# Kernel optimization log

Hardware: AMD Instinct MI355X
Metric: run time of the kernel (lower is better)

## Reference

```python
import jax, jax.numpy as jnp
import numpy as np

B, S, I, H, NC = 256, 1024, 64, 128, 10

def setup_inputs() -> dict:
    key = jax.random.key(0)
    ks = jax.random.split(key, 12)
    s_dh = 1.0 / np.sqrt(I)
    s_lstm = 1.0 / np.sqrt(H)
    return {
        "values": jax.random.normal(ks[0], (B, S, I), dtype=jnp.float32),
        "masks": jax.random.randint(ks[1], (B, S, I), 0, 2, dtype=jnp.int32),
        "deltas": jax.random.uniform(ks[2], (B, S, I), dtype=jnp.float32),
        "W_dh": jax.random.uniform(ks[3], (H, I), minval=-s_dh, maxval=s_dh),
        "b_dh": jax.random.uniform(ks[4], (H,), minval=-s_dh, maxval=s_dh),
        "W_dx": jax.random.uniform(ks[5], (I, I), minval=-s_dh, maxval=s_dh),
        "b_dx": jax.random.uniform(ks[6], (I,), minval=-s_dh, maxval=s_dh),
        "W_ih": jax.random.uniform(ks[7], (4 * H, 2 * I), minval=-s_lstm, maxval=s_lstm),
        "W_hh": jax.random.uniform(ks[8], (4 * H, H), minval=-s_lstm, maxval=s_lstm),
        "b_ih": jax.random.uniform(ks[9], (4 * H,), minval=-s_lstm, maxval=s_lstm),
        "b_hh": jax.random.uniform(ks[10], (4 * H,), minval=-s_lstm, maxval=s_lstm),
        "W_out": jax.random.uniform(ks[11], (NC, H), minval=-s_lstm, maxval=s_lstm),
        "b_out": jnp.zeros((NC,), dtype=jnp.float32),
    }

def _grud_forward(values, masks_f, deltas, W_dh, b_dh, W_dx, b_dx, W_ih, W_hh, b_ih, b_hh, W_out, b_out):
    eye = jnp.eye(W_dx.shape[0], dtype=W_dx.dtype)
    W_dx_diag = W_dx * eye  # TemporalDecay diag=True masks weight with identity

    def step(carry, xs):
        h, c = carry
        x, m, d = xs  # each (B, I)
        gamma_h = jnp.exp(-jax.nn.relu(d @ W_dh.T + b_dh))  # (B, H)
        gamma_x = jnp.exp(-jax.nn.relu(d @ W_dx_diag.T + b_dx))  # (B, I)
        h = h * gamma_h
        x_h = m * x + (1.0 - m) * (1.0 - gamma_x)  # forwards=None -> f = 1.0
        inp = jnp.concatenate([x_h, m], axis=1)  # (B, 2I)
        gates = inp @ W_ih.T + b_ih + h @ W_hh.T + b_hh  # (B, 4H)
        i_g, f_g, g_g, o_g = jnp.split(gates, 4, axis=1)
        c = jax.nn.sigmoid(f_g) * c + jax.nn.sigmoid(i_g) * jnp.tanh(g_g)
        h = jax.nn.sigmoid(o_g) * jnp.tanh(c)
        return (h, c), x_h

    b, _, _ = values.shape
    hdim = W_hh.shape[1]
    h0 = jnp.zeros((b, hdim), dtype=values.dtype)
    c0 = jnp.zeros((b, hdim), dtype=values.dtype)
    xs = (jnp.swapaxes(values, 0, 1), jnp.swapaxes(masks_f, 0, 1), jnp.swapaxes(deltas, 0, 1))
    (h, c), imputes = jax.lax.scan(step, (h0, c0), xs)
    impute_tensor = jnp.swapaxes(imputes, 0, 1)  # (B, S, I)
    y_h = h @ W_out.T + b_out  # dropout is identity in eval mode
    return y_h, impute_tensor

def reference(values, masks, deltas, W_dh, b_dh, W_dx, b_dx, W_ih, W_hh, b_ih, b_hh, W_out, b_out):
    masks_f = masks.astype(values.dtype)
    return _grud_forward(values, masks_f, deltas, W_dh, b_dh, W_dx, b_dx, W_ih, W_hh, b_ih, b_hh, W_out, b_out)
```

## Files before the change

### kernel.cpp

```cpp
#include <hip/hip_runtime.h>
#include <hip/hip_fp16.h>

#define NB   256
#define NS   1024
#define NI   64
#define NH   128
#define NCLS 10

typedef _Float16 h1;
typedef h1 h2 __attribute__((ext_vector_type(2)));
struct alignas(16) H8 { h2 v[4]; };

__device__ __forceinline__ h2 mk2(float a, float b) {
  h2 r; r[0] = (h1)a; r[1] = (h1)b; return r;
}

__device__ __forceinline__ float fdot2(h2 a, h2 b, float c) {
#if __has_builtin(__builtin_amdgcn_fdot2)
  return __builtin_amdgcn_fdot2(a, b, c, false);
#else
  return c + (float)a[0] * (float)b[0] + (float)a[1] * (float)b[1];
#endif
}

__device__ __forceinline__ float fast_rcp(float x) {
#if __has_builtin(__builtin_amdgcn_rcpf)
  return __builtin_amdgcn_rcpf(x);
#else
  return 1.0f / x;
#endif
}

__device__ __forceinline__ float tanh_f(float x) {
  return 2.f * fast_rcp(1.f + __expf(-2.f * x)) - 1.f;
}

__device__ __forceinline__ float sigm(float x) {
  return fast_rcp(1.f + __expf(-x));
}

template<int CTRL>
__device__ __forceinline__ float dpp_add(float x) {
  int y = __builtin_amdgcn_update_dpp(0, __float_as_int(x), CTRL, 0xF, 0xF, true);
  return x + __int_as_float(y);
}
__device__ __forceinline__ float red8(float x) {
  x = dpp_add<0xB1>(x);
  x = dpp_add<0x4E>(x);
  x = dpp_add<0x141>(x);
  return x;
}

__global__ __launch_bounds__(1024, 4) void grud_fused(
    const float* __restrict__ values,
    const int*   __restrict__ masks,
    const float* __restrict__ deltas,
    const float* __restrict__ W_dh, const float* __restrict__ b_dh,
    const float* __restrict__ W_dx, const float* __restrict__ b_dx,
    const float* __restrict__ W_ih, const float* __restrict__ W_hh,
    const float* __restrict__ b_ih, const float* __restrict__ b_hh,
    const float* __restrict__ W_out, const float* __restrict__ b_out,
    float* __restrict__ out)
{
  const int b   = blockIdx.x;
  const int tid = threadIdx.x;
  const int l   = tid & 63;
  const int w   = tid >> 6;
  const int q   = l & 7;
  const int g   = l >> 3;
  const int j   = (w << 3) | g;
  const int e0  = q << 5;

  __shared__ alignas(16) h1 opA[256];
  __shared__ alignas(16) h1 opB[256];
  __shared__ float hfin[NH];

  h2 wt0[16], wt1[16], wt2[16], wt3[16];
  {
    const size_t roff = (e0 < 128) ? (size_t)e0 : (size_t)(e0 - 128);
    const float* wbase = (e0 < 128) ? W_ih : W_hh;
#define LOADW(WT, R)                                                          \
    {                                                                         \
      const float4* w4 = reinterpret_cast<const float4*>(                     \
          wbase + ((size_t)((R) * NH + j)) * 128 + roff);                     \
      _Pragma("unroll")                                                       \
      for (int k = 0; k < 8; ++k) {                                           \
        float4 f = w4[k];                                                     \
        WT[2 * k]     = mk2(f.x, f.y);                                        \
        WT[2 * k + 1] = mk2(f.z, f.w);                                        \
      }                                                                       \
    }
    LOADW(wt0, 0) LOADW(wt1, 1) LOADW(wt2, 2) LOADW(wt3, 3)
#undef LOADW
  }
  const float bs0 = b_ih[j]            + b_hh[j];
  const float bs1 = b_ih[NH + j]       + b_hh[NH + j];
  const float bs2 = b_ih[2 * NH + j]   + b_hh[2 * NH + j];
  const float bs3 = b_ih[3 * NH + j]   + b_hh[3 * NH + j];
  h2 wd0, wd1, wd2, wd3;
  {
    const float4* a4 = reinterpret_cast<const float4*>(W_dh + j * 64 + q * 8);
    float4 f0 = a4[0], f1 = a4[1];
    wd0 = mk2(f0.x, f0.y); wd1 = mk2(f0.z, f0.w);
    wd2 = mk2(f1.x, f1.y); wd3 = mk2(f1.z, f1.w);
  }
  const float bdh = b_dh[j];
  float wdx_i = 0.f, bdx_i = 0.f;
  if (tid < NI) { wdx_i = W_dx[tid * 64 + tid]; bdx_i = b_dx[tid]; }

  const size_t base_b = (size_t)b * NS * NI;
  float* out_y   = out;
  float* out_imp = out + NB * NCLS;

  if (tid < NH) opA[128 + tid] = (h1)0.f;
  if (tid < NI) {
    float x0 = values[base_b + tid];
    float m0 = (float)masks[base_b + tid];
    float d0 = deltas[base_b + tid];
    float gx = __expf(-fmaxf(d0 * wdx_i + bdx_i, 0.f));
    float xh = m0 * x0 + (1.f - m0) * (1.f - gx);
    out_imp[base_b + tid] = xh;
    opA[tid]      = (h1)xh;
    opA[64 + tid] = (h1)m0;
  }

  h1* cur = opA;
  h1* nxt = opB;
  float c_st = 0.f, h_st = 0.f;

  for (int t = 0; t < NS; ++t) {
    __syncthreads();
    const int    tn = (t + 1 < NS) ? (t + 1) : (NS - 1);
    const size_t nb = base_b + (size_t)tn * NI;

    const float4* dn4 = reinterpret_cast<const float4*>(deltas + nb + q * 8);
    float4 pa = dn4[0], pb = dn4[1];
    float px = 0.f, pm = 0.f, pdv = 0.f;
    if (tid < NI) {
      px  = values[nb + tid];
      pm  = (float)masks[nb + tid];
      pdv = deltas[nb + tid];
    }

    const H8* s4 = reinterpret_cast<const H8*>(cur + e0);
    H8 o0 = s4[0], o1 = s4[1], o2 = s4[2], o3 = s4[3];

    float a0 = 0.f, a1 = 0.f, a2 = 0.f, a3 = 0.f;
#pragma unroll
    for (int p = 0; p < 4; ++p) {
      a0 = fdot2(o0.v[p], wt0[p], a0);
      a1 = fdot2(o0.v[p], wt1[p], a1);
      a2 = fdot2(o0.v[p], wt2[p], a2);
      a3 = fdot2(o0.v[p], wt3[p], a3);
    }
#pragma unroll
    for (int p = 0; p < 4; ++p) {
      a0 = fdot2(o1.v[p], wt0[4 + p], a0);
      a1 = fdot2(o1.v[p], wt1[4 + p], a1);
      a2 = fdot2(o1.v[p], wt2[4 + p], a2);
      a3 = fdot2(o1.v[p], wt3[4 + p], a3);
    }
#pragma unroll
    for (int p = 0; p < 4; ++p) {
      a0 = fdot2(o2.v[p], wt0[8 + p], a0);
      a1 = fdot2(o2.v[p], wt1[8 + p], a1);
      a2 = fdot2(o2.v[p], wt2[8 + p], a2);
      a3 = fdot2(o2.v[p], wt3[8 + p], a3);
    }
#pragma unroll
    for (int p = 0; p < 4; ++p) {
      a0 = fdot2(o3.v[p], wt0[12 + p], a0);
      a1 = fdot2(o3.v[p], wt1[12 + p], a1);
      a2 = fdot2(o3.v[p], wt2[12 + p], a2);
      a3 = fdot2(o3.v[p], wt3[12 + p], a3);
    }

    float gi = red8(a0) + bs0;
    float gf = red8(a1) + bs1;
    float gg = red8(a2) + bs2;
    float go = red8(a3) + bs3;

    float ia = sigm(gi);
    float fa = sigm(gf);
    float ga = tanh_f(gg);
    float oa = sigm(go);

    c_st = fa * c_st + ia * ga;
    h_st = oa * tanh_f(c_st);

    h2 p0 = mk2(pa.x, pa.y), p1 = mk2(pa.z, pa.w);
    h2 p2 = mk2(pb.x, pb.y), p3 = mk2(pb.z, pb.w);
    float part = fdot2(p3, wd3, fdot2(p2, wd2, fdot2(p1, wd1, fdot2(p0, wd0, 0.f))));
    part = red8(part);
    float gh = __expf(-fmaxf(part + bdh, 0.f));

    if (tid < NI) {
      float gx = __expf(-fmaxf(pdv * wdx_i + bdx_i, 0.f));
      float xh = pm * px + (1.f - pm) * (1.f - gx);
      if (t + 1 < NS) out_imp[nb + tid] = xh;
      nxt[tid]      = (h1)xh;
      nxt[64 + tid] = (h1)pm;
    }
    if (q == 0) nxt[128 + j] = (h1)(h_st * gh);

    h1* tmp = cur; cur = nxt; nxt = tmp;
  }

  if (q == 0) hfin[j] = h_st;
  __syncthreads();
  if (tid < NCLS) {
    float acc = b_out[tid];
    const float4* wo4 = reinterpret_cast<const float4*>(W_out + tid * NH);
#pragma unroll
    for (int k = 0; k < 32; ++k) {
      float4 a = wo4[k];
      acc += a.x * hfin[4 * k] + a.y * hfin[4 * k + 1] +
             a.z * hfin[4 * k + 2] + a.w * hfin[4 * k + 3];
    }
    out_y[b * NCLS + tid] = acc;
  }
}

extern "C" void kernel_launch(void* const* d_in, const int* in_sizes, int n_in,
                              void* d_out, int out_size, void* d_ws, size_t ws_size,
                              hipStream_t stream) {
  (void)in_sizes; (void)n_in; (void)d_ws; (void)ws_size; (void)out_size;
  grud_fused<<<dim3(NB), dim3(1024), 0, stream>>>(
      (const float*)d_in[0],  (const int*)d_in[1],   (const float*)d_in[2],
      (const float*)d_in[3],  (const float*)d_in[4], (const float*)d_in[5],
      (const float*)d_in[6],  (const float*)d_in[7], (const float*)d_in[8],
      (const float*)d_in[9],  (const float*)d_in[10],(const float*)d_in[11],
      (const float*)d_in[12], (float*)d_out);
}
```

Measured before the change: 1.503 ms.

## Split each hidden unit across 4 lanes with 512-thread blocks and padded LDS

Each hidden unit now uses 4 lanes instead of 8, so blocks shrink from 1024 to 512 threads. Each lane holds 128 fp16 weights across the four gates, and the cross-lane reduction drops to two DPP steps. The LDS operand buffer is padded to 72-element chunks to cut bank conflicts on the wider per-lane reads, and the float-to-half conversion now uses packed cvt_pkrtz. The longer per-lane dot-product chain and higher register use may offset the cheaper barriers and reductions.

```diff
diff --git a/kernel.cpp b/kernel.cpp
--- a/kernel.cpp
+++ b/kernel.cpp
@@ -11,8 +11,11 @@
 typedef h1 h2 __attribute__((ext_vector_type(2)));
 struct alignas(16) H8 { h2 v[4]; };
 
-__device__ __forceinline__ h2 mk2(float a, float b) {
-  h2 r; r[0] = (h1)a; r[1] = (h1)b; return r;
+#define CH_H1  72
+#define BUF_H1 (4 * CH_H1)
+
+__device__ __forceinline__ h2 pk(float a, float b) {
+  return __builtin_bit_cast(h2, __builtin_amdgcn_cvt_pkrtz(a, b));
 }
 
 __device__ __forceinline__ float fdot2(h2 a, h2 b, float c) {
@@ -34,7 +37,6 @@
 __device__ __forceinline__ float tanh_f(float x) {
   return 2.f * fast_rcp(1.f + __expf(-2.f * x)) - 1.f;
 }
-
 __device__ __forceinline__ float sigm(float x) {
   return fast_rcp(1.f + __expf(-x));
 }
@@ -44,14 +46,13 @@
   int y = __builtin_amdgcn_update_dpp(0, __float_as_int(x), CTRL, 0xF, 0xF, true);
   return x + __int_as_float(y);
 }
-__device__ __forceinline__ float red8(float x) {
+__device__ __forceinline__ float red4(float x) {
   x = dpp_add<0xB1>(x);
   x = dpp_add<0x4E>(x);
-  x = dpp_add<0x141>(x);
   return x;
 }
 
-__global__ __launch_bounds__(1024, 4) void grud_fused(
+__global__ __launch_bounds__(512, 2) void grud_fused(
     const float* __restrict__ values,
     const int*   __restrict__ masks,
     const float* __restrict__ deltas,
@@ -66,45 +67,42 @@
   const int tid = threadIdx.x;
   const int l   = tid & 63;
   const int w   = tid >> 6;
-  const int q   = l & 7;
-  const int g   = l >> 3;
-  const int j   = (w << 3) | g;
-  const int e0  = q << 5;
-
-  __shared__ alignas(16) h1 opA[256];
-  __shared__ alignas(16) h1 opB[256];
+  const int q   = l & 3;
+  const int u   = (w << 4) | (l >> 2);
+
+  __shared__ alignas(16) h1 opA[BUF_H1];
+  __shared__ alignas(16) h1 opB[BUF_H1];
   __shared__ float hfin[NH];
 
-  h2 wt0[16], wt1[16], wt2[16], wt3[16];
+  h2 wt[4][32];
+#pragma unroll
+  for (int g = 0; g < 4; ++g) {
+    const int row = g * NH + u;
+    const float* src = (q < 2) ? (W_ih + (size_t)row * 128 + 64 * q)
+                               : (W_hh + (size_t)row * 128 + 64 * (q - 2));
+    const float4* s4 = reinterpret_cast<const float4*>(src);
+#pragma unroll
+    for (int k = 0; k < 16; ++k) {
+      float4 f = s4[k];
+      wt[g][2 * k]     = pk(f.x, f.y);
+      wt[g][2 * k + 1] = pk(f.z, f.w);
+    }
+  }
+  const float bs0 = 0.25f * (b_ih[u]          + b_hh[u]);
+  const float bs1 = 0.25f * (b_ih[NH + u]     + b_hh[NH + u]);
+  const float bs2 = 0.25f * (b_ih[2 * NH + u] + b_hh[2 * NH + u]);
+  const float bs3 = 0.25f * (b_ih[3 * NH + u] + b_hh[3 * NH + u]);
+  h2 wdh[8];
   {
-    const size_t roff = (e0 < 128) ? (size_t)e0 : (size_t)(e0 - 128);
-    const float* wbase = (e0 < 128) ? W_ih : W_hh;
-#define LOADW(WT, R)                                                          \
-    {                                                                         \
-      const float4* w4 = reinterpret_cast<const float4*>(                     \
-          wbase + ((size_t)((R) * NH + j)) * 128 + roff);                     \
-      _Pragma("unroll")                                                       \
-      for (int k = 0; k < 8; ++k) {                                           \
-        float4 f = w4[k];                                                     \
-        WT[2 * k]     = mk2(f.x, f.y);                                        \
-        WT[2 * k + 1] = mk2(f.z, f.w);                                        \
-      }                                                                       \
-    }
-    LOADW(wt0, 0) LOADW(wt1, 1) LOADW(wt2, 2) LOADW(wt3, 3)
-#undef LOADW
-  }
-  const float bs0 = b_ih[j]            + b_hh[j];
-  const float bs1 = b_ih[NH + j]       + b_hh[NH + j];
-  const float bs2 = b_ih[2 * NH + j]   + b_hh[2 * NH + j];
-  const float bs3 = b_ih[3 * NH + j]   + b_hh[3 * NH + j];
-  h2 wd0, wd1, wd2, wd3;
-  {
-    const float4* a4 = reinterpret_cast<const float4*>(W_dh + j * 64 + q * 8);
-    float4 f0 = a4[0], f1 = a4[1];
-    wd0 = mk2(f0.x, f0.y); wd1 = mk2(f0.z, f0.w);
-    wd2 = mk2(f1.x, f1.y); wd3 = mk2(f1.z, f1.w);
-  }
-  const float bdh = b_dh[j];
+    const float4* a4 = reinterpret_cast<const float4*>(W_dh + u * 64 + 16 * q);
+#pragma unroll
+    for (int k = 0; k < 4; ++k) {
+      float4 f = a4[k];
+      wdh[2 * k]     = pk(f.x, f.y);
+      wdh[2 * k + 1] = pk(f.z, f.w);
+    }
+  }
+  const float bdh4 = 0.25f * b_dh[u];
   float wdx_i = 0.f, bdx_i = 0.f;
   if (tid < NI) { wdx_i = W_dx[tid * 64 + tid]; bdx_i = b_dx[tid]; }
 
@@ -112,7 +110,10 @@
   float* out_y   = out;
   float* out_imp = out + NB * NCLS;
 
-  if (tid < NH) opA[128 + tid] = (h1)0.f;
+  if (tid < NH) {
+    int e = 128 + tid;
+    opA[CH_H1 * (e >> 6) + (e & 63)] = (h1)0.f;
+  }
   if (tid < NI) {
     float x0 = values[base_b + tid];
     float m0 = (float)masks[base_b + tid];
@@ -120,8 +121,8 @@
     float gx = __expf(-fmaxf(d0 * wdx_i + bdx_i, 0.f));
     float xh = m0 * x0 + (1.f - m0) * (1.f - gx);
     out_imp[base_b + tid] = xh;
-    opA[tid]      = (h1)xh;
-    opA[64 + tid] = (h1)m0;
+    opA[tid]         = (h1)xh;
+    opA[CH_H1 + tid] = (h1)m0;
   }
 
   h1* cur = opA;
@@ -133,8 +134,8 @@
     const int    tn = (t + 1 < NS) ? (t + 1) : (NS - 1);
     const size_t nb = base_b + (size_t)tn * NI;
 
-    const float4* dn4 = reinterpret_cast<const float4*>(deltas + nb + q * 8);
-    float4 pa = dn4[0], pb = dn4[1];
+    const float4* dn4 = reinterpret_cast<const float4*>(deltas + nb + 16 * q);
+    float4 pd0 = dn4[0], pd1 = dn4[1], pd2 = dn4[2], pd3 = dn4[3];
     float px = 0.f, pm = 0.f, pdv = 0.f;
     if (tid < NI) {
       px  = values[nb + tid];
@@ -142,43 +143,27 @@
       pdv = deltas[nb + tid];
     }
 
-    const H8* s4 = reinterpret_cast<const H8*>(cur + e0);
-    H8 o0 = s4[0], o1 = s4[1], o2 = s4[2], o3 = s4[3];
-
-    float a0 = 0.f, a1 = 0.f, a2 = 0.f, a3 = 0.f;
-#pragma unroll
-    for (int p = 0; p < 4; ++p) {
-      a0 = fdot2(o0.v[p], wt0[p], a0);
-      a1 = fdot2(o0.v[p], wt1[p], a1);
-      a2 = fdot2(o0.v[p], wt2[p], a2);
-      a3 = fdot2(o0.v[p], wt3[p], a3);
-    }
-#pragma unroll
-    for (int p = 0; p < 4; ++p) {
-      a0 = fdot2(o1.v[p], wt0[4 + p], a0);
-      a1 = fdot2(o1.v[p], wt1[4 + p], a1);
-      a2 = fdot2(o1.v[p], wt2[4 + p], a2);
-      a3 = fdot2(o1.v[p], wt3[4 + p], a3);
-    }
-#pragma unroll
-    for (int p = 0; p < 4; ++p) {
-      a0 = fdot2(o2.v[p], wt0[8 + p], a0);
-      a1 = fdot2(o2.v[p], wt1[8 + p], a1);
-      a2 = fdot2(o2.v[p], wt2[8 + p], a2);
-      a3 = fdot2(o2.v[p], wt3[8 + p], a3);
-    }
-#pragma unroll
-    for (int p = 0; p < 4; ++p) {
-      a0 = fdot2(o3.v[p], wt0[12 + p], a0);
-      a1 = fdot2(o3.v[p], wt1[12 + p], a1);
-      a2 = fdot2(o3.v[p], wt2[12 + p], a2);
-      a3 = fdot2(o3.v[p], wt3[12 + p], a3);
-    }
-
-    float gi = red8(a0) + bs0;
-    float gf = red8(a1) + bs1;
-    float gg = red8(a2) + bs2;
-    float go = red8(a3) + bs3;
+    const H8* s8 = reinterpret_cast<const H8*>(cur + CH_H1 * q);
+    H8 o[8];
+#pragma unroll
+    for (int p = 0; p < 8; ++p) o[p] = s8[p];
+
+    float a0 = bs0, a1 = bs1, a2 = bs2, a3 = bs3;
+#pragma unroll
+    for (int p = 0; p < 8; ++p) {
+#pragma unroll
+      for (int v = 0; v < 4; ++v) {
+        a0 = fdot2(o[p].v[v], wt[0][4 * p + v], a0);
+        a1 = fdot2(o[p].v[v], wt[1][4 * p + v], a1);
+        a2 = fdot2(o[p].v[v], wt[2][4 * p + v], a2);
+        a3 = fdot2(o[p].v[v], wt[3][4 * p + v], a3);
+      }
+    }
+
+    float gi = red4(a0);
+    float gf = red4(a1);
+    float gg = red4(a2);
+    float go = red4(a3);
 
     float ia = sigm(gi);
     float fa = sigm(gf);
@@ -188,25 +173,38 @@
     c_st = fa * c_st + ia * ga;
     h_st = oa * tanh_f(c_st);
 
-    h2 p0 = mk2(pa.x, pa.y), p1 = mk2(pa.z, pa.w);
-    h2 p2 = mk2(pb.x, pb.y), p3 = mk2(pb.z, pb.w);
-    float part = fdot2(p3, wd3, fdot2(p2, wd2, fdot2(p1, wd1, fdot2(p0, wd0, 0.f))));
-    part = red8(part);
-    float gh = __expf(-fmaxf(part + bdh, 0.f));
+    h2 p0 = pk(pd0.x, pd0.y), p1 = pk(pd0.z, pd0.w);
+    h2 p2 = pk(pd1.x, pd1.y), p3 = pk(pd1.z, pd1.w);
+    h2 p4 = pk(pd2.x, pd2.y), p5 = pk(pd2.z, pd2.w);
+    h2 p6 = pk(pd3.x, pd3.y), p7 = pk(pd3.z, pd3.w);
+    float part = bdh4;
+    part = fdot2(p0, wdh[0], part);
+    part = fdot2(p1, wdh[1], part);
+    part = fdot2(p2, wdh[2], part);
+    part = fdot2(p3, wdh[3], part);
+    part = fdot2(p4, wdh[4], part);
+    part = fdot2(p5, wdh[5], part);
+    part = fdot2(p6, wdh[6], part);
+    part = fdot2(p7, wdh[7], part);
+    part = red4(part);
+    float gh = __expf(-fmaxf(part, 0.f));
 
     if (tid < NI) {
       float gx = __expf(-fmaxf(pdv * wdx_i + bdx_i, 0.f));
       float xh = pm * px + (1.f - pm) * (1.f - gx);
       if (t + 1 < NS) out_imp[nb + tid] = xh;
-      nxt[tid]      = (h1)xh;
-      nxt[64 + tid] = (h1)pm;
-    }
-    if (q == 0) nxt[128 + j] = (h1)(h_st * gh);
+      nxt[tid]         = (h1)xh;
+      nxt[CH_H1 + tid] = (h1)pm;
+    }
+    if (q == 0) {
+      int e = 128 + u;
+      nxt[CH_H1 * (e >> 6) + (e & 63)] = (h1)(h_st * gh);
+    }
 
     h1* tmp = cur; cur = nxt; nxt = tmp;
   }
 
-  if (q == 0) hfin[j] = h_st;
+  if (q == 0) hfin[u] = h_st;
   __syncthreads();
   if (tid < NCLS) {
     float acc = b_out[tid];
@@ -225,7 +223,7 @@
                               void* d_out, int out_size, void* d_ws, size_t ws_size,
                               hipStream_t stream) {
   (void)in_sizes; (void)n_in; (void)d_ws; (void)ws_size; (void)out_size;
-  grud_fused<<<dim3(NB), dim3(1024), 0, stream>>>(
+  grud_fused<<<dim3(NB), dim3(512), 0, stream>>>(
       (const float*)d_in[0],  (const int*)d_in[1],   (const float*)d_in[2],
       (const float*)d_in[3],  (const float*)d_in[4], (const float*)d_in[5],
       (const float*)d_in[6],  (const float*)d_in[7], (const float*)d_in[8],
```

After: 1.594 ms. 1.06x slower.
